# Optimization experiments

Measured on AMD Instinct MI355X. Metric: run time of the kernel, lower is better.

The kernel has to match this reference:

```python
import jax, jax.numpy as jnp
import numpy as np

N = 50000   # nodes
E = 150000  # edges
G = 256     # graphs in batch
H0, H1, H2, H3 = 8, 128, 256, 512


def _lin(key, fi, fo):
    return jax.random.normal(key, (fi, fo), dtype=jnp.float32) * (1.0 / np.sqrt(fi))


def setup_inputs() -> dict:
    key = jax.random.key(0)
    ks = jax.random.split(key, 12)
    x = jax.random.normal(ks[0], (N, H0), dtype=jnp.float32)
    edge_index = jax.random.randint(ks[1], (2, E), 0, N)
    edge_weight = jax.random.uniform(ks[2], (E,), dtype=jnp.float32)
    batch = jnp.sort(jax.random.randint(ks[3], (N,), 0, G))
    return {
        'x': x, 'edge_index': edge_index, 'edge_weight': edge_weight, 'batch': batch,
        'W1': _lin(ks[4], H0, H1), 'b1': jnp.zeros((H1,), jnp.float32),
        'W2': _lin(ks[5], H1, H2), 'b2': jnp.zeros((H2,), jnp.float32),
        'W3': _lin(ks[6], H2, H3), 'b3': jnp.zeros((H3,), jnp.float32),
        'Wfc': _lin(ks[7], H3, 1), 'bfc': jnp.zeros((1,), jnp.float32),
    }


def _gcn_conv(h, W, b, src, dst, ew, n):
    # h: [N, Fin] -> [N, Fout]; symmetric GCN normalization (self-loops already in src/dst/ew)
    h = h @ W                                             # [N, Fout]
    deg = jax.ops.segment_sum(ew, dst, num_segments=n)    # [N]
    dinv = jnp.where(deg > 0, jax.lax.rsqrt(deg), 0.0)
    norm = dinv[src] * ew * dinv[dst]                     # [E+N]
    msgs = h[src] * norm[:, None]                         # gather + scale
    out = jax.ops.segment_sum(msgs, dst, num_segments=n)  # scatter-add
    return out + b


def reference(x, edge_index, edge_weight, batch, W1, b1, W2, b2, W3, b3, Wfc, bfc):
    n = x.shape[0]
    loop = jnp.arange(n)
    src = jnp.concatenate([edge_index[0], loop])
    dst = jnp.concatenate([edge_index[1], loop])
    ew = jnp.concatenate([edge_weight, jnp.ones((n,), edge_weight.dtype)])

    h1 = jax.nn.relu(_gcn_conv(x, W1, b1, src, dst, ew, n))
    h2 = jax.nn.relu(_gcn_conv(h1, W2, b2, src, dst, ew, n))
    h3 = jax.nn.relu(_gcn_conv(h2, W3, b3, src, dst, ew, n))

    # global mean pool over graphs
    sums = jax.ops.segment_sum(h3, batch, num_segments=G)              # [G, H3]
    cnt = jax.ops.segment_sum(jnp.ones((n,), h3.dtype), batch, num_segments=G)
    pooled = sums / jnp.maximum(cnt, 1.0)[:, None]

    return jax.nn.sigmoid(pooled @ Wfc + bfc)              # [G, 1]
```

## Files before the change

### kernel.cpp

```cpp
#include <hip/hip_runtime.h>
#include <math.h>

typedef __attribute__((ext_vector_type(8))) short short8;
typedef __attribute__((ext_vector_type(4))) float floatx4;


__device__ __forceinline__ unsigned short f2bf(float f) {
    unsigned int u = __float_as_uint(f);
    unsigned int r = (u + 0x7fffu + ((u >> 16) & 1u)) >> 16;
    return (unsigned short)r;
}
__device__ __forceinline__ float bfu_lo(unsigned int u) {
    return __uint_as_float(u << 16);
}
__device__ __forceinline__ float bfu_hi(unsigned int u) {
    return __uint_as_float(u & 0xffff0000u);
}


__global__ void k_init(float* __restrict__ deg, int* __restrict__ cnt,
                       int* __restrict__ cursor, int N) {
    int i = blockIdx.x * blockDim.x + threadIdx.x;
    if (i < N) { deg[i] = 1.0f; cnt[i] = 0; cursor[i] = 0; }
}

__global__ void k_hist_deg(const int* __restrict__ dst, const float* __restrict__ ew,
                           float* __restrict__ deg, int* __restrict__ cnt, int E) {
    int e = blockIdx.x * blockDim.x + threadIdx.x;
    if (e < E) {
        int d = dst[e];
        atomicAdd(&deg[d], ew[e]);
        atomicAdd(&cnt[d], 1);
    }
}

__global__ void k_dinv(float* __restrict__ deg, int N) {
    int i = blockIdx.x * blockDim.x + threadIdx.x;
    if (i < N) deg[i] = rsqrtf(deg[i]);
}

__global__ void k_norm(const int* __restrict__ src, const int* __restrict__ dst,
                       const float* __restrict__ ew, const float* __restrict__ dinv,
                       float* __restrict__ norm, int E) {
    int e = blockIdx.x * blockDim.x + threadIdx.x;
    if (e < E) norm[e] = dinv[src[e]] * ew[e] * dinv[dst[e]];
}


__global__ __launch_bounds__(256) void k_scan_a(const int* __restrict__ cnt,
                                                int* __restrict__ bsum, int N) {
    int b = blockIdx.x, t = threadIdx.x;
    int base = b * 1024 + t * 4;
    int s = 0;
#pragma unroll
    for (int j = 0; j < 4; ++j) { int i = base + j; if (i < N) s += cnt[i]; }
    __shared__ int sh[256];
    sh[t] = s; __syncthreads();
    for (int st = 128; st > 0; st >>= 1) { if (t < st) sh[t] += sh[t + st]; __syncthreads(); }
    if (t == 0) bsum[b] = sh[0];
}

__global__ __launch_bounds__(256) void k_scan_b(int* __restrict__ bsum, int nb) {
    int t = threadIdx.x;
    __shared__ int sh[256];
    int orig = (t < nb) ? bsum[t] : 0;
    sh[t] = orig; __syncthreads();
    for (int off = 1; off < 256; off <<= 1) {
        int x = (t >= off) ? sh[t - off] : 0;
        __syncthreads();
        sh[t] += x;
        __syncthreads();
    }
    if (t < nb) bsum[t] = sh[t] - orig;
}

__global__ __launch_bounds__(256) void k_scan_c(const int* __restrict__ cnt,
                                                const int* __restrict__ boff,
                                                int* __restrict__ row_start, int N) {
    int b = blockIdx.x, t = threadIdx.x;
    int base = b * 1024 + t * 4;
    int v[4]; int s = 0;
#pragma unroll
    for (int j = 0; j < 4; ++j) { int i = base + j; v[j] = (i < N) ? cnt[i] : 0; s += v[j]; }
    __shared__ int sh[256];
    sh[t] = s; __syncthreads();
    for (int off = 1; off < 256; off <<= 1) {
        int x = (t >= off) ? sh[t - off] : 0;
        __syncthreads();
        sh[t] += x;
        __syncthreads();
    }
    int excl = sh[t] - s + boff[b];
#pragma unroll
    for (int j = 0; j < 4; ++j) {
        int i = base + j;
        if (i < N) row_start[i] = excl;
        excl += v[j];
        if (i == N - 1) row_start[N] = excl;
    }
}

__global__ void k_scatter(const int* __restrict__ src, const int* __restrict__ dst,
                          const float* __restrict__ nrm, const int* __restrict__ row_start,
                          int* __restrict__ cursor, int* __restrict__ esrc,
                          float* __restrict__ enorm, int E) {
    int e = blockIdx.x * blockDim.x + threadIdx.x;
    if (e >= E) return;
    int d = dst[e];
    int pos = row_start[d] + atomicAdd(&cursor[d], 1);
    esrc[pos] = src[e];
    enorm[pos] = nrm[e];
}


__global__ void k_agg_f32(const float* __restrict__ h, const float* __restrict__ dinv,
                          const int* __restrict__ esrc, const float* __restrict__ enorm,
                          const int* __restrict__ row_start, float* __restrict__ out,
                          int N, int shiftF, int maskF) {
    int gid = blockIdx.x * blockDim.x + threadIdx.x;
    if (gid >= (N << shiftF)) return;
    int n = gid >> shiftF;
    int f = gid & maskF;
    float dv = dinv[n];
    float acc = h[gid] * dv * dv;
    int s0 = row_start[n], s1 = row_start[n + 1];
    for (int j = s0; j < s1; ++j)
        acc += enorm[j] * h[((size_t)esrc[j] << shiftF) | f];
    out[gid] = acc;
}


__global__ void k_agg_bf(const unsigned short* __restrict__ h, const float* __restrict__ dinv,
                         const int* __restrict__ esrc, const float* __restrict__ enorm,
                         const int* __restrict__ row_start,
                         unsigned short* __restrict__ A,
                         int N, int Mpad, int F, int qsh) {
    int p = blockIdx.x * blockDim.x + threadIdx.x;
    int quart = F >> 2;
    if (p >= Mpad * quart) return;
    int n = p >> qsh;
    int fq = (p & (quart - 1)) << 2;
    size_t oidx = (size_t)n * F + fq;
    if (n >= N) {
        *(ushort4*)&A[oidx] = make_ushort4(0, 0, 0, 0);
        return;
    }
    float dv = dinv[n];
    float dv2 = dv * dv;
    uint2 hv = *(const uint2*)&h[oidx];
    float s0 = bfu_lo(hv.x) * dv2, s1 = bfu_hi(hv.x) * dv2;
    float s2 = bfu_lo(hv.y) * dv2, s3 = bfu_hi(hv.y) * dv2;
    int j0 = row_start[n], j1 = row_start[n + 1];
    for (int j = j0; j < j1; ++j) {
        int s = esrc[j];
        float w = enorm[j];
        uint2 nv = *(const uint2*)&h[(size_t)s * F + fq];
        s0 += w * bfu_lo(nv.x);
        s1 += w * bfu_hi(nv.x);
        s2 += w * bfu_lo(nv.y);
        s3 += w * bfu_hi(nv.y);
    }
    *(ushort4*)&A[oidx] = make_ushort4(f2bf(s0), f2bf(s1), f2bf(s2), f2bf(s3));
}


__global__ void k_wt_bf(const float* __restrict__ W, unsigned short* __restrict__ WT,
                        int K, int Fout) {
    int gid = blockIdx.x * blockDim.x + threadIdx.x;
    if (gid >= K * Fout) return;
    int k = gid / Fout, n = gid % Fout;
    WT[(size_t)n * K + k] = f2bf(W[gid]);
}


template <int EPI>
__global__ __launch_bounds__(256, 4) void k_gemm_async(
    const unsigned short* __restrict__ A, const unsigned short* __restrict__ B,
    const float* __restrict__ bias, unsigned short* __restrict__ C,
    const float* __restrict__ Wfc, float* __restrict__ part,
    int M, int Mpad, int K, int Fout, int nbsh) {
    __shared__ __align__(16) unsigned short smem[8192];

    int tid = threadIdx.x, wave = tid >> 6, lane = tid & 63;
    int quad = lane >> 4, r = lane & 15;

    int P = blockIdx.x;
    int r8 = P & 7;
    int q = P >> 3;
    int bnIdx = q & ((1 << nbsh) - 1);
    int g = ((q >> nbsh) << 3) + r8;
    int bm = g * 128, bn = bnIdx * 128;
    int wm = (wave & 1) * 64, wn = (wave >> 1) * 64;

    const unsigned short* gsrc[2] = {A, B};
    const int rb[2] = {bm, bn};

    floatx4 acc[4][4] = {};

    for (int k0 = 0; k0 < K; k0 += 32) {
#pragma unroll
        for (int t = 0; t < 2; ++t) {
#pragma unroll
            for (int i = 0; i < 2; ++i) {
                int qc = wave * 2 + i;
                int idx = qc * 64 + lane;
                int row = idx >> 2, kofs = (idx & 3) << 3;
                const unsigned short* gptr = gsrc[t] + ((size_t)(rb[t] + row) * K + k0 + kofs);
                unsigned short* l = &smem[t * 4096 + qc * 512];
                __builtin_amdgcn_global_load_lds(
                    (const __attribute__((address_space(1))) void*)gptr,
                    (__attribute__((address_space(3))) void*)l, 16, 0, 0);
            }
        }
        __syncthreads();

        short8 ah[4];
#pragma unroll
        for (int mt = 0; mt < 4; ++mt) {
            int m = wm + mt * 16 + r;
            ah[mt] = *(const short8*)&smem[m * 32 + quad * 8];
        }
#pragma unroll
        for (int nt = 0; nt < 4; ++nt) {
            int n = wn + nt * 16 + r;
            short8 bh = *(const short8*)&smem[4096 + n * 32 + quad * 8];
#pragma unroll
            for (int mt = 0; mt < 4; ++mt)
                acc[mt][nt] = __builtin_amdgcn_mfma_f32_16x16x32_bf16(ah[mt], bh, acc[mt][nt], 0, 0, 0);
        }
        __syncthreads();
    }

    float bv[4];
#pragma unroll
    for (int nt = 0; nt < 4; ++nt) bv[nt] = bias[bn + wn + nt * 16 + r];

    if (EPI == 0) {
        float* eps = (float*)&smem[0] + wave * 1024;
#pragma unroll
        for (int mt = 0; mt < 4; ++mt) {
#pragma unroll
            for (int nt = 0; nt < 4; ++nt)
#pragma unroll
                for (int reg = 0; reg < 4; ++reg)
                    eps[(quad * 4 + reg) * 64 + nt * 16 + r] =
                        fmaxf(acc[mt][nt][reg] + bv[nt], 0.f);
#pragma unroll
            for (int i = 0; i < 4; ++i) {
                int fl = i * 64 + lane;
                int ri = fl >> 4, c4 = fl & 15;
                float4 v = *(const float4*)&eps[ri * 64 + c4 * 4];
                int gm = bm + wm + mt * 16 + ri;
                if (gm < M)
                    *(ushort4*)&C[(size_t)gm * Fout + bn + wn + c4 * 4] =
                        make_ushort4(f2bf(v.x), f2bf(v.y), f2bf(v.z), f2bf(v.w));
            }
        }
    } else {
        float* rowsum = (float*)&smem[0];
        if (tid < 128) rowsum[tid] = 0.f;
        __syncthreads();
        float wf[4];
#pragma unroll
        for (int nt = 0; nt < 4; ++nt) wf[nt] = Wfc[bn + wn + nt * 16 + r];
#pragma unroll
        for (int mt = 0; mt < 4; ++mt)
#pragma unroll
            for (int reg = 0; reg < 4; ++reg) {
                float v = 0.f;
#pragma unroll
                for (int nt = 0; nt < 4; ++nt)
                    v += fmaxf(acc[mt][nt][reg] + bv[nt], 0.f) * wf[nt];
                v += __shfl_xor(v, 1);
                v += __shfl_xor(v, 2);
                v += __shfl_xor(v, 4);
                v += __shfl_xor(v, 8);
                if (r == 0) atomicAdd(&rowsum[wm + mt * 16 + quad * 4 + reg], v);
            }
        __syncthreads();
        if (tid < 128) part[(size_t)bnIdx * Mpad + bm + tid] = rowsum[tid];
    }
}


template <int BK>
__global__ __launch_bounds__(256) void k_gemm_bias_relu(
    const float* __restrict__ A, const float* __restrict__ W,
    const float* __restrict__ bias, unsigned short* __restrict__ C,
    int M, int K, int Fout) {
    const int BM = 128, BN = 128;
    __shared__ float As[BK][BM + 4];
    __shared__ float Bs[BK][BN];

    int bm = blockIdx.x * BM;
    int bn = blockIdx.y * BN;
    int tid = threadIdx.x;
    int tx = tid & 15;
    int ty = tid >> 4;

    float acc[8][8];
#pragma unroll
    for (int i = 0; i < 8; ++i)
#pragma unroll
        for (int j = 0; j < 8; ++j) acc[i][j] = 0.f;

    for (int k0 = 0; k0 < K; k0 += BK) {
#pragma unroll
        for (int i = tid; i < BM * BK; i += 256) {
            int k = i % BK;
            int m = i / BK;
            int gm = bm + m;
            As[k][m] = (gm < M) ? A[(long long)gm * K + k0 + k] : 0.f;
        }
#pragma unroll
        for (int i = tid; i < BK * BN; i += 256) {
            int n = i % BN;
            int k = i / BN;
            Bs[k][n] = W[(long long)(k0 + k) * Fout + bn + n];
        }
        __syncthreads();

#pragma unroll
        for (int k = 0; k < BK; ++k) {
            float a[8], b[8];
            float4 a0 = *(const float4*)&As[k][ty * 4];
            float4 a1 = *(const float4*)&As[k][ty * 4 + 64];
            float4 b0 = *(const float4*)&Bs[k][tx * 4];
            float4 b1 = *(const float4*)&Bs[k][tx * 4 + 64];
            a[0] = a0.x; a[1] = a0.y; a[2] = a0.z; a[3] = a0.w;
            a[4] = a1.x; a[5] = a1.y; a[6] = a1.z; a[7] = a1.w;
            b[0] = b0.x; b[1] = b0.y; b[2] = b0.z; b[3] = b0.w;
            b[4] = b1.x; b[5] = b1.y; b[6] = b1.z; b[7] = b1.w;
#pragma unroll
            for (int i = 0; i < 8; ++i)
#pragma unroll
                for (int j = 0; j < 8; ++j) acc[i][j] += a[i] * b[j];
        }
        __syncthreads();
    }

    float4 bi0 = *(const float4*)&bias[bn + tx * 4];
    float4 bi1 = *(const float4*)&bias[bn + tx * 4 + 64];
    float bb[8] = {bi0.x, bi0.y, bi0.z, bi0.w, bi1.x, bi1.y, bi1.z, bi1.w};
#pragma unroll
    for (int i = 0; i < 8; ++i) {
        int gm = bm + ((i < 4) ? (ty * 4 + i) : (64 + ty * 4 + i - 4));
        if (gm >= M) continue;
        ushort4 v0, v1;
        v0.x = f2bf(fmaxf(acc[i][0] + bb[0], 0.f));
        v0.y = f2bf(fmaxf(acc[i][1] + bb[1], 0.f));
        v0.z = f2bf(fmaxf(acc[i][2] + bb[2], 0.f));
        v0.w = f2bf(fmaxf(acc[i][3] + bb[3], 0.f));
        v1.x = f2bf(fmaxf(acc[i][4] + bb[4], 0.f));
        v1.y = f2bf(fmaxf(acc[i][5] + bb[5], 0.f));
        v1.z = f2bf(fmaxf(acc[i][6] + bb[6], 0.f));
        v1.w = f2bf(fmaxf(acc[i][7] + bb[7], 0.f));
        *(ushort4*)&C[(long long)gm * Fout + bn + tx * 4] = v0;
        *(ushort4*)&C[(long long)gm * Fout + bn + tx * 4 + 64] = v1;
    }
}


__global__ __launch_bounds__(256) void k_pool2(const float* __restrict__ part,
                                               const int* __restrict__ batch,
                                               const float* __restrict__ bfc,
                                               float* __restrict__ out,
                                               int N, int Mpad, int nchunks, int G) {
    int g = (int)((blockIdx.x * blockDim.x + threadIdx.x) >> 6);
    int lane = threadIdx.x & 63;
    if (g >= G) return;
    int lo = 0, hi = N;
    while (lo < hi) { int m = (lo + hi) >> 1; if (batch[m] < g) lo = m + 1; else hi = m; }
    int start = lo;
    hi = N;
    while (lo < hi) { int m = (lo + hi) >> 1; if (batch[m] < g + 1) lo = m + 1; else hi = m; }
    int end = lo;
    float s = 0.f;
    for (int i = start + lane; i < end; i += 64) {
        float t = 0.f;
        for (int c = 0; c < nchunks; ++c) t += part[(size_t)c * Mpad + i];
        s += t;
    }
#pragma unroll
    for (int off = 32; off > 0; off >>= 1) s += __shfl_down(s, off);
    if (lane == 0) {
        float c = (float)(end - start);
        if (c < 1.f) c = 1.f;
        float z = s / c + bfc[0];
        out[g] = 1.f / (1.f + expf(-z));
    }
}


static inline int cdiv(int a, int b) { return (a + b - 1) / b; }

extern "C" void kernel_launch(void* const* d_in, const int* in_sizes, int n_in,
                              void* d_out, int out_size, void* d_ws, size_t ws_size,
                              hipStream_t stream) {
    const float* x   = (const float*)d_in[0];
    const int*   ei  = (const int*)d_in[1];
    const float* ew  = (const float*)d_in[2];
    const int*   bat = (const int*)d_in[3];
    const float* W1  = (const float*)d_in[4];
    const float* b1  = (const float*)d_in[5];
    const float* W2  = (const float*)d_in[6];
    const float* b2  = (const float*)d_in[7];
    const float* W3  = (const float*)d_in[8];
    const float* b3  = (const float*)d_in[9];
    const float* Wfc = (const float*)d_in[10];
    const float* bfc = (const float*)d_in[11];
    float* out = (float*)d_out;

    const int N  = in_sizes[3];
    const int E  = in_sizes[2];
    const int H0 = in_sizes[0] / N;
    const int H1 = in_sizes[5];
    const int H2 = in_sizes[7];
    const int H3 = in_sizes[9];
    const int G  = out_size;
    const int Mpad = cdiv(N, 1024) * 1024;
    const int Npad4 = (N + 4) & ~3;

    const int* srcv = ei;
    const int* dstv = ei + E;

    char* p = (char*)d_ws;
    float* dinv      = (float*)p; p += (size_t)N * 4;
    float* nrm       = (float*)p; p += (size_t)E * 4;
    int*   cnt       = (int*)p;   p += (size_t)N * 4;
    int*   cursor    = (int*)p;   p += (size_t)N * 4;
    int*   bsum      = (int*)p;   p += 256 * 4;
    int*   row_start = (int*)p;   p += (size_t)Npad4 * 4;
    int*   esrc      = (int*)p;   p += (size_t)E * 4;
    float* enorm     = (float*)p; p += (size_t)E * 4;
    float* part      = (float*)p; p += (size_t)(H3 / 128) * Mpad * 4;
    unsigned short* WT2 = (unsigned short*)p; p += (size_t)H1 * H2 * 2;
    unsigned short* WT3 = (unsigned short*)p; p += (size_t)H2 * H3 * 2;
    unsigned short* Abf = (unsigned short*)p; p += (size_t)Mpad * H2 * 2;
    unsigned short* h1  = (unsigned short*)p; p += (size_t)Mpad * H1 * 2;
    unsigned short* h2  = (unsigned short*)p; p += (size_t)Mpad * H2 * 2;
    float* aggP = (float*)p;      p += (size_t)N * H0 * 4;

    k_init<<<cdiv(N, 256), 256, 0, stream>>>(dinv, cnt, cursor, N);
    k_hist_deg<<<cdiv(E, 256), 256, 0, stream>>>(dstv, ew, dinv, cnt, E);
    k_dinv<<<cdiv(N, 256), 256, 0, stream>>>(dinv, N);
    k_norm<<<cdiv(E, 256), 256, 0, stream>>>(srcv, dstv, ew, dinv, nrm, E);

    int nb = cdiv(N, 1024);
    k_scan_a<<<nb, 256, 0, stream>>>(cnt, bsum, N);
    k_scan_b<<<1, 256, 0, stream>>>(bsum, nb);
    k_scan_c<<<nb, 256, 0, stream>>>(cnt, bsum, row_start, N);
    k_scatter<<<cdiv(E, 256), 256, 0, stream>>>(srcv, dstv, nrm, row_start, cursor, esrc, enorm, E);

    k_wt_bf<<<cdiv(H1 * H2, 256), 256, 0, stream>>>(W2, WT2, H1, H2);
    k_wt_bf<<<cdiv(H2 * H3, 256), 256, 0, stream>>>(W3, WT3, H2, H3);

    {
        int sh = __builtin_ctz(H0);
        k_agg_f32<<<cdiv(N << sh, 256), 256, 0, stream>>>(x, dinv, esrc, enorm, row_start,
                                                          aggP, N, sh, H0 - 1);
        dim3 grid(cdiv(N, 128), H1 / 128);
        k_gemm_bias_relu<8><<<grid, 256, 0, stream>>>(aggP, W1, b1, h1, N, H0, H1);
    }
    {
        k_agg_bf<<<cdiv(Mpad * (H1 / 4), 256), 256, 0, stream>>>(
            h1, dinv, esrc, enorm, row_start, Abf, N, Mpad, H1, __builtin_ctz(H1) - 2);
        int nbsh = __builtin_ctz(H2 / 128);
        k_gemm_async<0><<<(Mpad / 128) * (H2 / 128), 256, 0, stream>>>(
            Abf, WT2, b2, h2, nullptr, nullptr, N, Mpad, H1, H2, nbsh);
    }
    {
        k_agg_bf<<<cdiv(Mpad * (H2 / 4), 256), 256, 0, stream>>>(
            h2, dinv, esrc, enorm, row_start, Abf, N, Mpad, H2, __builtin_ctz(H2) - 2);
        int nbsh = __builtin_ctz(H3 / 128);
        k_gemm_async<1><<<(Mpad / 128) * (H3 / 128), 256, 0, stream>>>(
            Abf, WT3, b3, nullptr, Wfc, part, N, Mpad, H2, H3, nbsh);
    }

    k_pool2<<<cdiv(G * 64, 256), 256, 0, stream>>>(part, bat, bfc, out, N, Mpad, H3 / 128, G);
}
```

Before: 240.8 us.

## Fuse preprocessing kernels and merge layer-1 aggregation with its small GEMM

Folds the rsqrt of the degree into the first scan pass, computes the edge norm inside the CSR scatter so the separate norm array goes away, merges the two weight-transpose launches into one, and replaces the layer-1 fp32 aggregation plus tiled GEMM with a single kernel. That kernel gives each wavefront one node, which aggregates the 8 input features and multiplies by W1 held in shared memory. Fewer launches and no intermediate aggPre/nrm round trips through memory are the goal. The trade-off is that every wave walks the same edge list redundantly across lanes, and each block reloads W1 into shared memory.

```diff
diff --git a/kernel.cpp b/kernel.cpp
--- a/kernel.cpp
+++ b/kernel.cpp
@@ -34,26 +34,17 @@
     }
 }
 
-__global__ void k_dinv(float* __restrict__ deg, int N) {
-    int i = blockIdx.x * blockDim.x + threadIdx.x;
-    if (i < N) deg[i] = rsqrtf(deg[i]);
-}
-
-__global__ void k_norm(const int* __restrict__ src, const int* __restrict__ dst,
-                       const float* __restrict__ ew, const float* __restrict__ dinv,
-                       float* __restrict__ norm, int E) {
-    int e = blockIdx.x * blockDim.x + threadIdx.x;
-    if (e < E) norm[e] = dinv[src[e]] * ew[e] * dinv[dst[e]];
-}
-
-
-__global__ __launch_bounds__(256) void k_scan_a(const int* __restrict__ cnt,
-                                                int* __restrict__ bsum, int N) {
+__global__ __launch_bounds__(256) void k_dinv_scana(float* __restrict__ deg,
+                                                    const int* __restrict__ cnt,
+                                                    int* __restrict__ bsum, int N) {
     int b = blockIdx.x, t = threadIdx.x;
     int base = b * 1024 + t * 4;
     int s = 0;
 #pragma unroll
-    for (int j = 0; j < 4; ++j) { int i = base + j; if (i < N) s += cnt[i]; }
+    for (int j = 0; j < 4; ++j) {
+        int i = base + j;
+        if (i < N) { deg[i] = rsqrtf(deg[i]); s += cnt[i]; }
+    }
     __shared__ int sh[256];
     sh[t] = s; __syncthreads();
     for (int st = 128; st > 0; st >>= 1) { if (t < st) sh[t] += sh[t + st]; __syncthreads(); }
@@ -100,33 +91,80 @@
     }
 }
 
-__global__ void k_scatter(const int* __restrict__ src, const int* __restrict__ dst,
-                          const float* __restrict__ nrm, const int* __restrict__ row_start,
-                          int* __restrict__ cursor, int* __restrict__ esrc,
-                          float* __restrict__ enorm, int E) {
+__global__ void k_scatter_norm(const int* __restrict__ src, const int* __restrict__ dst,
+                               const float* __restrict__ ew, const float* __restrict__ dinv,
+                               const int* __restrict__ row_start, int* __restrict__ cursor,
+                               int* __restrict__ esrc, float* __restrict__ enorm, int E) {
     int e = blockIdx.x * blockDim.x + threadIdx.x;
     if (e >= E) return;
-    int d = dst[e];
+    int d = dst[e], s = src[e];
     int pos = row_start[d] + atomicAdd(&cursor[d], 1);
-    esrc[pos] = src[e];
-    enorm[pos] = nrm[e];
-}
-
-
-__global__ void k_agg_f32(const float* __restrict__ h, const float* __restrict__ dinv,
-                          const int* __restrict__ esrc, const float* __restrict__ enorm,
-                          const int* __restrict__ row_start, float* __restrict__ out,
-                          int N, int shiftF, int maskF) {
+    esrc[pos] = s;
+    enorm[pos] = dinv[s] * ew[e] * dinv[d];
+}
+
+
+__global__ void k_wt_all(const float* __restrict__ W2, unsigned short* __restrict__ WT2,
+                         int K2, int F2,
+                         const float* __restrict__ W3, unsigned short* __restrict__ WT3,
+                         int K3, int F3) {
     int gid = blockIdx.x * blockDim.x + threadIdx.x;
-    if (gid >= (N << shiftF)) return;
-    int n = gid >> shiftF;
-    int f = gid & maskF;
+    int n2 = K2 * F2;
+    if (gid < n2) {
+        int k = gid / F2, n = gid % F2;
+        WT2[(size_t)n * K2 + k] = f2bf(W2[gid]);
+    } else {
+        gid -= n2;
+        if (gid >= K3 * F3) return;
+        int k = gid / F3, n = gid % F3;
+        WT3[(size_t)n * K3 + k] = f2bf(W3[gid]);
+    }
+}
+
+
+__global__ __launch_bounds__(256) void k_l1(
+    const float* __restrict__ x, const float* __restrict__ dinv,
+    const int* __restrict__ esrc, const float* __restrict__ enorm,
+    const int* __restrict__ row_start, const float* __restrict__ W1,
+    const float* __restrict__ b1, unsigned short* __restrict__ h1, int N) {
+    __shared__ float w1s[1024];
+    __shared__ float b1s[128];
+    int tid = threadIdx.x;
+#pragma unroll
+    for (int i = tid; i < 1024; i += 256) w1s[i] = W1[i];
+    if (tid < 128) b1s[tid] = b1[tid];
+    __syncthreads();
+
+    int wave = tid >> 6, lane = tid & 63;
+    int n = blockIdx.x * 4 + wave;
+    if (n >= N) return;
+
     float dv = dinv[n];
-    float acc = h[gid] * dv * dv;
-    int s0 = row_start[n], s1 = row_start[n + 1];
-    for (int j = s0; j < s1; ++j)
-        acc += enorm[j] * h[((size_t)esrc[j] << shiftF) | f];
-    out[gid] = acc;
+    float dv2 = dv * dv;
+    float a[8];
+    float4 v0 = *(const float4*)&x[(size_t)n * 8];
+    float4 v1 = *(const float4*)&x[(size_t)n * 8 + 4];
+    a[0] = v0.x * dv2; a[1] = v0.y * dv2; a[2] = v0.z * dv2; a[3] = v0.w * dv2;
+    a[4] = v1.x * dv2; a[5] = v1.y * dv2; a[6] = v1.z * dv2; a[7] = v1.w * dv2;
+
+    int j0 = row_start[n], j1 = row_start[n + 1];
+    for (int j = j0; j < j1; ++j) {
+        int s = esrc[j];
+        float w = enorm[j];
+        float4 u0 = *(const float4*)&x[(size_t)s * 8];
+        float4 u1 = *(const float4*)&x[(size_t)s * 8 + 4];
+        a[0] += w * u0.x; a[1] += w * u0.y; a[2] += w * u0.z; a[3] += w * u0.w;
+        a[4] += w * u1.x; a[5] += w * u1.y; a[6] += w * u1.z; a[7] += w * u1.w;
+    }
+
+    float acc0 = b1s[lane], acc1 = b1s[lane + 64];
+#pragma unroll
+    for (int k = 0; k < 8; ++k) {
+        acc0 += a[k] * w1s[k * 128 + lane];
+        acc1 += a[k] * w1s[k * 128 + lane + 64];
+    }
+    h1[(size_t)n * 128 + lane] = f2bf(fmaxf(acc0, 0.f));
+    h1[(size_t)n * 128 + lane + 64] = f2bf(fmaxf(acc1, 0.f));
 }
 
 
@@ -164,15 +202,6 @@
 }
 
 
-__global__ void k_wt_bf(const float* __restrict__ W, unsigned short* __restrict__ WT,
-                        int K, int Fout) {
-    int gid = blockIdx.x * blockDim.x + threadIdx.x;
-    if (gid >= K * Fout) return;
-    int k = gid / Fout, n = gid % Fout;
-    WT[(size_t)n * K + k] = f2bf(W[gid]);
-}
-
-
 template <int EPI>
 __global__ __launch_bounds__(256, 4) void k_gemm_async(
     const unsigned short* __restrict__ A, const unsigned short* __restrict__ B,
@@ -279,84 +308,6 @@
             }
         __syncthreads();
         if (tid < 128) part[(size_t)bnIdx * Mpad + bm + tid] = rowsum[tid];
-    }
-}
-
-
-template <int BK>
-__global__ __launch_bounds__(256) void k_gemm_bias_relu(
-    const float* __restrict__ A, const float* __restrict__ W,
-    const float* __restrict__ bias, unsigned short* __restrict__ C,
-    int M, int K, int Fout) {
-    const int BM = 128, BN = 128;
-    __shared__ float As[BK][BM + 4];
-    __shared__ float Bs[BK][BN];
-
-    int bm = blockIdx.x * BM;
-    int bn = blockIdx.y * BN;
-    int tid = threadIdx.x;
-    int tx = tid & 15;
-    int ty = tid >> 4;
-
-    float acc[8][8];
-#pragma unroll
-    for (int i = 0; i < 8; ++i)
-#pragma unroll
-        for (int j = 0; j < 8; ++j) acc[i][j] = 0.f;
-
-    for (int k0 = 0; k0 < K; k0 += BK) {
-#pragma unroll
-        for (int i = tid; i < BM * BK; i += 256) {
-            int k = i % BK;
-            int m = i / BK;
-            int gm = bm + m;
-            As[k][m] = (gm < M) ? A[(long long)gm * K + k0 + k] : 0.f;
-        }
-#pragma unroll
-        for (int i = tid; i < BK * BN; i += 256) {
-            int n = i % BN;
-            int k = i / BN;
-            Bs[k][n] = W[(long long)(k0 + k) * Fout + bn + n];
-        }
-        __syncthreads();
-
-#pragma unroll
-        for (int k = 0; k < BK; ++k) {
-            float a[8], b[8];
-            float4 a0 = *(const float4*)&As[k][ty * 4];
-            float4 a1 = *(const float4*)&As[k][ty * 4 + 64];
-            float4 b0 = *(const float4*)&Bs[k][tx * 4];
-            float4 b1 = *(const float4*)&Bs[k][tx * 4 + 64];
-            a[0] = a0.x; a[1] = a0.y; a[2] = a0.z; a[3] = a0.w;
-            a[4] = a1.x; a[5] = a1.y; a[6] = a1.z; a[7] = a1.w;
-            b[0] = b0.x; b[1] = b0.y; b[2] = b0.z; b[3] = b0.w;
-            b[4] = b1.x; b[5] = b1.y; b[6] = b1.z; b[7] = b1.w;
-#pragma unroll
-            for (int i = 0; i < 8; ++i)
-#pragma unroll
-                for (int j = 0; j < 8; ++j) acc[i][j] += a[i] * b[j];
-        }
-        __syncthreads();
-    }
-
-    float4 bi0 = *(const float4*)&bias[bn + tx * 4];
-    float4 bi1 = *(const float4*)&bias[bn + tx * 4 + 64];
-    float bb[8] = {bi0.x, bi0.y, bi0.z, bi0.w, bi1.x, bi1.y, bi1.z, bi1.w};
-#pragma unroll
-    for (int i = 0; i < 8; ++i) {
-        int gm = bm + ((i < 4) ? (ty * 4 + i) : (64 + ty * 4 + i - 4));
-        if (gm >= M) continue;
-        ushort4 v0, v1;
-        v0.x = f2bf(fmaxf(acc[i][0] + bb[0], 0.f));
-        v0.y = f2bf(fmaxf(acc[i][1] + bb[1], 0.f));
-        v0.z = f2bf(fmaxf(acc[i][2] + bb[2], 0.f));
-        v0.w = f2bf(fmaxf(acc[i][3] + bb[3], 0.f));
-        v1.x = f2bf(fmaxf(acc[i][4] + bb[4], 0.f));
-        v1.y = f2bf(fmaxf(acc[i][5] + bb[5], 0.f));
-        v1.z = f2bf(fmaxf(acc[i][6] + bb[6], 0.f));
-        v1.w = f2bf(fmaxf(acc[i][7] + bb[7], 0.f));
-        *(ushort4*)&C[(long long)gm * Fout + bn + tx * 4] = v0;
-        *(ushort4*)&C[(long long)gm * Fout + bn + tx * 4 + 64] = v1;
     }
 }
 
@@ -413,7 +364,6 @@
 
     const int N  = in_sizes[3];
     const int E  = in_sizes[2];
-    const int H0 = in_sizes[0] / N;
     const int H1 = in_sizes[5];
     const int H2 = in_sizes[7];
     const int H3 = in_sizes[9];
@@ -426,7 +376,6 @@
 
     char* p = (char*)d_ws;
     float* dinv      = (float*)p; p += (size_t)N * 4;
-    float* nrm       = (float*)p; p += (size_t)E * 4;
     int*   cnt       = (int*)p;   p += (size_t)N * 4;
     int*   cursor    = (int*)p;   p += (size_t)N * 4;
     int*   bsum      = (int*)p;   p += 256 * 4;
@@ -439,43 +388,29 @@
     unsigned short* Abf = (unsigned short*)p; p += (size_t)Mpad * H2 * 2;
     unsigned short* h1  = (unsigned short*)p; p += (size_t)Mpad * H1 * 2;
     unsigned short* h2  = (unsigned short*)p; p += (size_t)Mpad * H2 * 2;
-    float* aggP = (float*)p;      p += (size_t)N * H0 * 4;
 
     k_init<<<cdiv(N, 256), 256, 0, stream>>>(dinv, cnt, cursor, N);
     k_hist_deg<<<cdiv(E, 256), 256, 0, stream>>>(dstv, ew, dinv, cnt, E);
-    k_dinv<<<cdiv(N, 256), 256, 0, stream>>>(dinv, N);
-    k_norm<<<cdiv(E, 256), 256, 0, stream>>>(srcv, dstv, ew, dinv, nrm, E);
-
     int nb = cdiv(N, 1024);
-    k_scan_a<<<nb, 256, 0, stream>>>(cnt, bsum, N);
+    k_dinv_scana<<<nb, 256, 0, stream>>>(dinv, cnt, bsum, N);
     k_scan_b<<<1, 256, 0, stream>>>(bsum, nb);
     k_scan_c<<<nb, 256, 0, stream>>>(cnt, bsum, row_start, N);
-    k_scatter<<<cdiv(E, 256), 256, 0, stream>>>(srcv, dstv, nrm, row_start, cursor, esrc, enorm, E);
-
-    k_wt_bf<<<cdiv(H1 * H2, 256), 256, 0, stream>>>(W2, WT2, H1, H2);
-    k_wt_bf<<<cdiv(H2 * H3, 256), 256, 0, stream>>>(W3, WT3, H2, H3);
-
-    {
-        int sh = __builtin_ctz(H0);
-        k_agg_f32<<<cdiv(N << sh, 256), 256, 0, stream>>>(x, dinv, esrc, enorm, row_start,
-                                                          aggP, N, sh, H0 - 1);
-        dim3 grid(cdiv(N, 128), H1 / 128);
-        k_gemm_bias_relu<8><<<grid, 256, 0, stream>>>(aggP, W1, b1, h1, N, H0, H1);
-    }
-    {
-        k_agg_bf<<<cdiv(Mpad * (H1 / 4), 256), 256, 0, stream>>>(
-            h1, dinv, esrc, enorm, row_start, Abf, N, Mpad, H1, __builtin_ctz(H1) - 2);
-        int nbsh = __builtin_ctz(H2 / 128);
-        k_gemm_async<0><<<(Mpad / 128) * (H2 / 128), 256, 0, stream>>>(
-            Abf, WT2, b2, h2, nullptr, nullptr, N, Mpad, H1, H2, nbsh);
-    }
-    {
-        k_agg_bf<<<cdiv(Mpad * (H2 / 4), 256), 256, 0, stream>>>(
-            h2, dinv, esrc, enorm, row_start, Abf, N, Mpad, H2, __builtin_ctz(H2) - 2);
-        int nbsh = __builtin_ctz(H3 / 128);
-        k_gemm_async<1><<<(Mpad / 128) * (H3 / 128), 256, 0, stream>>>(
-            Abf, WT3, b3, nullptr, Wfc, part, N, Mpad, H2, H3, nbsh);
-    }
+    k_scatter_norm<<<cdiv(E, 256), 256, 0, stream>>>(srcv, dstv, ew, dinv, row_start,
+                                                     cursor, esrc, enorm, E);
+
+    k_wt_all<<<cdiv(H1 * H2 + H2 * H3, 256), 256, 0, stream>>>(W2, WT2, H1, H2, W3, WT3, H2, H3);
+
+    k_l1<<<cdiv(N, 4), 256, 0, stream>>>(x, dinv, esrc, enorm, row_start, W1, b1, h1, N);
+
+    k_agg_bf<<<cdiv(Mpad * (H1 / 4), 256), 256, 0, stream>>>(
+        h1, dinv, esrc, enorm, row_start, Abf, N, Mpad, H1, __builtin_ctz(H1) - 2);
+    k_gemm_async<0><<<(Mpad / 128) * (H2 / 128), 256, 0, stream>>>(
+        Abf, WT2, b2, h2, nullptr, nullptr, N, Mpad, H1, H2, __builtin_ctz(H2 / 128));
+
+    k_agg_bf<<<cdiv(Mpad * (H2 / 4), 256), 256, 0, stream>>>(
+        h2, dinv, esrc, enorm, row_start, Abf, N, Mpad, H2, __builtin_ctz(H2) - 2);
+    k_gemm_async<1><<<(Mpad / 128) * (H3 / 128), 256, 0, stream>>>(
+        Abf, WT3, b3, nullptr, Wfc, part, N, Mpad, H2, H3, __builtin_ctz(H3 / 128));
 
     k_pool2<<<cdiv(G * 64, 256), 256, 0, stream>>>(part, bat, bfc, out, N, Mpad, H3 / 128, G);
 }
```

Result: slower. 251.9 us (+4.6%).
